# Kernel tuning notes

Measured on AMD Instinct MI355X. Metric: run time of the kernel, lower is better.

The kernel has to match this reference:

```python
import jax, jax.numpy as jnp
import numpy as np

B, S, H = 4, 2048, 1024

def setup_inputs() -> dict:
    key = jax.random.key(0)
    ks = jax.random.split(key, 7)
    scale = 1.0 / np.sqrt(H)
    x  = jax.random.normal(ks[0], (B, S, H), dtype=jnp.float32)
    Wq = jax.random.normal(ks[1], (H, H), dtype=jnp.float32) * scale
    bq = jax.random.normal(ks[2], (H,), dtype=jnp.float32) * 0.01
    Wk = jax.random.normal(ks[3], (H, H), dtype=jnp.float32) * scale
    bk = jax.random.normal(ks[4], (H,), dtype=jnp.float32) * 0.01
    Wv = jax.random.normal(ks[5], (H, H), dtype=jnp.float32) * scale
    bv = jax.random.normal(ks[6], (H,), dtype=jnp.float32) * 0.01
    return {"x": x, "Wq": Wq, "bq": bq, "Wk": Wk, "bk": bk, "Wv": Wv, "bv": bv}

def reference(x, Wq, bq, Wk, bk, Wv, bv):
    # q/k/v: [B, S, H]
    q = jnp.einsum('bsh,hd->bsd', x, Wq.T) + bq
    k = jnp.einsum('bsh,hd->bsd', x, Wk.T) + bk
    v = jnp.einsum('bsh,hd->bsd', x, Wv.T) + bv
    # NOTE: original module applies NO 1/sqrt(H) scaling.
    scores = jnp.einsum('bqd,bkd->bqk', q, k)  # [B, S, S]
    attn = jax.nn.softmax(scores, axis=-1)
    return jnp.einsum('bqk,bkd->bqd', attn, v)  # [B, S, H]
```

## Files before the change

kernel.cpp:

```cpp
#include <hip/hip_runtime.h>
#include <hip/hip_bf16.h>


typedef __attribute__((ext_vector_type(4))) float f32x4;
typedef __attribute__((ext_vector_type(16))) float f32x16;
typedef __attribute__((ext_vector_type(8))) _Float16 f16x8;
typedef __attribute__((ext_vector_type(4))) unsigned short us4;
typedef __attribute__((ext_vector_type(8))) unsigned short us8;

#define MFMA16F(a, b, c) __builtin_amdgcn_mfma_f32_16x16x32_f16((a), (b), (c), 0, 0, 0)
#define MFMA32F(a, b, c) __builtin_amdgcn_mfma_f32_32x32x16_f16((a), (b), (c), 0, 0, 0)

static __device__ __forceinline__ unsigned short f2h_u(float x) {
  _Float16 h = (_Float16)x;
  return *reinterpret_cast<unsigned short*>(&h);
}
static __device__ __forceinline__ float hu2f(unsigned short u) {
  _Float16 h;
  *reinterpret_cast<unsigned short*>(&h) = u;
  return (float)h;
}

__global__ __launch_bounds__(256) void split_x_kernel(
    const float* __restrict__ in, unsigned short* __restrict__ outp, int ntiles) {
  const int t = blockIdx.x * 256 + threadIdx.x;
  if (t >= ntiles * 64) return;
  const int tile = t >> 6;
  const int l = t & 63;
  const int m = (tile >> 5) * 16 + (l & 15);
  const int kb = (tile & 31) * 32 + (l >> 4) * 8;
  const float* src = in + (size_t)m * 1024 + kb;
  f32x4 v0 = *(const f32x4*)src;
  f32x4 v1 = *(const f32x4*)(src + 4);
  us8 h;
#pragma unroll
  for (int j = 0; j < 4; j++) {
    h[j] = f2h_u(v0[j]);
    h[j + 4] = f2h_u(v1[j]);
  }
  *(us8*)(outp + (size_t)tile * 512 + l * 8) = h;
}

__global__ __launch_bounds__(256) void split3_kernel(
    const float* __restrict__ w0, const float* __restrict__ w1,
    const float* __restrict__ w2,
    unsigned short* __restrict__ h0, unsigned short* __restrict__ l0,
    unsigned short* __restrict__ h1, unsigned short* __restrict__ l1,
    unsigned short* __restrict__ h2, unsigned short* __restrict__ l2) {
  const int which = blockIdx.y;
  const float* in = which == 0 ? w0 : (which == 1 ? w1 : w2);
  unsigned short* hi = which == 0 ? h0 : (which == 1 ? h1 : h2);
  unsigned short* lo = which == 0 ? l0 : (which == 1 ? l1 : l2);
  const int t = blockIdx.x * 256 + threadIdx.x;
  const int tile = t >> 6;
  const int l = t & 63;
  const int m = (tile >> 5) * 16 + (l & 15);
  const int kb = (tile & 31) * 32 + (l >> 4) * 8;
  const float* src = in + (size_t)m * 1024 + kb;
  f32x4 v0 = *(const f32x4*)src;
  f32x4 v1 = *(const f32x4*)(src + 4);
  us8 h, lv;
#pragma unroll
  for (int j = 0; j < 4; j++) {
    unsigned short hu = f2h_u(v0[j]);
    h[j] = hu;
    lv[j] = f2h_u(v0[j] - hu2f(hu));
    hu = f2h_u(v1[j]);
    h[j + 4] = hu;
    lv[j + 4] = f2h_u(v1[j] - hu2f(hu));
  }
  *(us8*)(hi + (size_t)tile * 512 + l * 8) = h;
  if (which != 2) *(us8*)(lo + (size_t)tile * 512 + l * 8) = lv;
}

__global__ __launch_bounds__(256, 2) void proj_fused_kernel(
    const unsigned short* __restrict__ Xf,
    const unsigned short* __restrict__ Wqh, const unsigned short* __restrict__ Wql,
    const unsigned short* __restrict__ Wkh, const unsigned short* __restrict__ Wkl,
    const unsigned short* __restrict__ Wvh,
    const float* __restrict__ bq, const float* __restrict__ bk,
    const float* __restrict__ bv,
    unsigned short* __restrict__ Qf, unsigned short* __restrict__ Kf,
    unsigned short* __restrict__ Vt) {
  const int tid = threadIdx.x;
  const int lane = tid & 63;
  const int wid = tid >> 6;
  const int lrow = lane & 15;
  const int kg = lane >> 4;
  const int bx = blockIdx.x;
  const int ntb = blockIdx.y * 16 + wid * 4;
  const int z = blockIdx.z;

  const unsigned short* Wh = z == 0 ? Wqh : (z == 1 ? Wkh : Wvh);
  const unsigned short* Wl = z == 0 ? Wql : Wkl;
  const float* bias = z == 0 ? bq : (z == 1 ? bk : bv);

  const unsigned short* xf = Xf + (size_t)(bx * 8) * 32 * 512 + lane * 8;

  f32x4 acc[8][4];
#pragma unroll
  for (int mf = 0; mf < 8; mf++)
#pragma unroll
    for (int cf = 0; cf < 4; cf++) acc[mf][cf] = f32x4{0.f, 0.f, 0.f, 0.f};

  if (z < 2) {
    for (int kt = 0; kt < 32; kt++) {
      const size_t o = (size_t)kt * 512;
      f16x8 ah[8];
#pragma unroll
      for (int mf = 0; mf < 8; mf++)
        ah[mf] = *(const f16x8*)(xf + (size_t)mf * 32 * 512 + o);
#pragma unroll
      for (int cf = 0; cf < 4; cf++) {
        const size_t wo = ((size_t)(ntb + cf) * 32 + kt) * 512 + lane * 8;
        f16x8 bh = *(const f16x8*)(Wh + wo);
        f16x8 bl = *(const f16x8*)(Wl + wo);
#pragma unroll
        for (int mf = 0; mf < 8; mf++) {
          acc[mf][cf] = MFMA16F(ah[mf], bh, acc[mf][cf]);
          acc[mf][cf] = MFMA16F(ah[mf], bl, acc[mf][cf]);
        }
      }
    }
    unsigned short* O = z == 0 ? Qf : Kf;
    const int b = bx >> 4;
#pragma unroll
    for (int mf = 0; mf < 8; mf++) {
      const int s0 = (bx & 15) * 128 + mf * 16 + kg * 4;
#pragma unroll
      for (int cf = 0; cf < 4; cf++) {
        const int nt = ntb + cf;
        const float bv_ = bias[nt * 16 + lrow];
#pragma unroll
        for (int i = 0; i < 4; i++) {
          const int s = s0 + i;
          const size_t a = ((size_t)((b * 64 + (s >> 5)) * 64 + nt)) * 512 +
                           (s & 31) * 16 + lrow;
          O[a] = f2h_u(acc[mf][cf][i] + bv_);
        }
      }
    }
  } else {
    for (int kt = 0; kt < 32; kt++) {
      const size_t o = (size_t)kt * 512;
      f16x8 ah[8];
#pragma unroll
      for (int mf = 0; mf < 8; mf++)
        ah[mf] = *(const f16x8*)(xf + (size_t)mf * 32 * 512 + o);
#pragma unroll
      for (int cf = 0; cf < 4; cf++) {
        const size_t wo = ((size_t)(ntb + cf) * 32 + kt) * 512 + lane * 8;
        f16x8 bh = *(const f16x8*)(Wh + wo);
#pragma unroll
        for (int mf = 0; mf < 8; mf++) acc[mf][cf] = MFMA16F(ah[mf], bh, acc[mf][cf]);
      }
    }
    const int b = bx >> 4;
#pragma unroll
    for (int mf = 0; mf < 8; mf++) {
      const int kl_hi = (bx & 15) * 8 + mf;
#pragma unroll
      for (int cf = 0; cf < 4; cf++) {
        const int d = (ntb + cf) * 16 + lrow;
        const float bv_ = bias[d];
        us4 pk;
#pragma unroll
        for (int i = 0; i < 4; i++) pk[i] = f2h_u(acc[mf][cf][i] + bv_);
        const size_t a = ((size_t)(b * 32 + (d >> 5)) * 128 + kl_hi) * 512 +
                         (size_t)(d & 31) * 16 + kg * 4;
        *reinterpret_cast<us4*>(&Vt[a]) = pk;
      }
    }
  }
}

__global__ __launch_bounds__(1024, 4) void attn_kernel(
    const unsigned short* __restrict__ Qf, const unsigned short* __restrict__ Kf,
    const unsigned short* __restrict__ Vt, float* __restrict__ out) {
  __shared__ unsigned short LDSB[65536];
  __shared__ float redM[16][32];
  __shared__ float redS[16][32];
  __shared__ float rowinv[32];

  const int tid = threadIdx.x;
  const int lane = tid & 63;
  const int wid = tid >> 6;
  const int lq = lane & 31;
  const int hi = lane >> 5;
  const int lo16 = lq * 16 + hi * 8;

  const int id = blockIdx.x;
  const int xcd = id & 7;
  const int b = xcd >> 1;
  const int qt = (xcd & 1) + ((id >> 3) << 1);
  const int q0 = qt * 32;

  {
    const unsigned short* qsrc = Qf + ((size_t)(b * 64 + qt) * 64) * 512;
#pragma unroll
    for (int i = 0; i < 4; i++) {
      const int idx = (i * 1024 + tid) * 8;
      *(us8*)&LDSB[idx] = *(const us8*)&qsrc[idx];
    }
  }
  __syncthreads();

  f32x16 acc0, acc1, acc2, acc3;
#pragma unroll
  for (int r = 0; r < 16; r++) { acc0[r] = 0.f; acc1[r] = 0.f; acc2[r] = 0.f; acc3[r] = 0.f; }

  const unsigned short* kb = Kf + ((size_t)(b * 64 + wid * 4) * 64) * 512 + lo16;
#define KLD(G, KKK) (*(const f16x8*)(kb + (size_t)(G)*64 * 512 + (size_t)(KKK)*512))
  f16x8 kc0 = KLD(0, 0), kc1 = KLD(1, 0), kc2 = KLD(2, 0), kc3 = KLD(3, 0);
  for (int kk = 0; kk < 63; kk++) {
    f16x8 q = *(const f16x8*)&LDSB[kk * 512 + lo16];
    f16x8 kn0 = KLD(0, kk + 1), kn1 = KLD(1, kk + 1),
          kn2 = KLD(2, kk + 1), kn3 = KLD(3, kk + 1);
    __builtin_amdgcn_s_setprio(1);
    acc0 = MFMA32F(kc0, q, acc0);
    acc1 = MFMA32F(kc1, q, acc1);
    acc2 = MFMA32F(kc2, q, acc2);
    acc3 = MFMA32F(kc3, q, acc3);
    __builtin_amdgcn_s_setprio(0);
    kc0 = kn0; kc1 = kn1; kc2 = kn2; kc3 = kn3;
  }
  {
    f16x8 q = *(const f16x8*)&LDSB[63 * 512 + lo16];
    acc0 = MFMA32F(kc0, q, acc0);
    acc1 = MFMA32F(kc1, q, acc1);
    acc2 = MFMA32F(kc2, q, acc2);
    acc3 = MFMA32F(kc3, q, acc3);
  }
#undef KLD

  float m = -3.0e38f;
#pragma unroll
  for (int r = 0; r < 16; r++) {
    m = fmaxf(m, fmaxf(fmaxf(acc0[r], acc1[r]), fmaxf(acc2[r], acc3[r])));
  }
  m = fmaxf(m, __shfl_xor(m, 32));
  if (hi == 0) redM[wid][lq] = m;
  __syncthreads();
  float M = redM[0][lq];
#pragma unroll
  for (int w = 1; w < 16; w++) M = fmaxf(M, redM[w][lq]);

  float s = 0.f;
#pragma unroll
  for (int r = 0; r < 16; r++) {
    acc0[r] = __expf(acc0[r] - M); s += acc0[r];
    acc1[r] = __expf(acc1[r] - M); s += acc1[r];
    acc2[r] = __expf(acc2[r] - M); s += acc2[r];
    acc3[r] = __expf(acc3[r] - M); s += acc3[r];
  }
  s += __shfl_xor(s, 32);
  if (hi == 0) redS[wid][lq] = s;
  __syncthreads();
  if (tid < 32) {
    float ss = 0.f;
#pragma unroll
    for (int w = 0; w < 16; w++) ss += redS[w][tid];
    rowinv[tid] = 1.0f / ss;
  }

  const int swz = (lq & 7) << 3;
  const int pb = lq * 2048 + wid * 128 + 4 * hi;
#define PWRITE(GG, ACC)                                                     \
  {                                                                         \
    _Pragma("unroll")                                                       \
    for (int qd = 0; qd < 4; qd++) {                                        \
      us4 pk;                                                               \
      _Pragma("unroll")                                                     \
      for (int i = 0; i < 4; i++) pk[i] = f2h_u(ACC[qd * 4 + i]);           \
      *(us4*)&LDSB[(pb + (GG)*32 + qd * 8) ^ swz] = pk;                     \
    }                                                                       \
  }
  PWRITE(0, acc0)
  PWRITE(1, acc1)
  PWRITE(2, acc2)
  PWRITE(3, acc3)
#undef PWRITE
  __syncthreads();

  f32x16 o0, o1;
#pragma unroll
  for (int r = 0; r < 16; r++) { o0[r] = 0.f; o1[r] = 0.f; }

  const unsigned short* vt0 = Vt + ((size_t)(b * 32 + wid * 2) * 128) * 512 + lo16;
  const unsigned short* vt1 = vt0 + (size_t)128 * 512;
  const int prow = lq * 2048 + hi * 8;
#define VLD(P, KKK) (*(const f16x8*)((P) + (size_t)(KKK)*512))
  f16x8 vc0 = VLD(vt0, 0), vc1 = VLD(vt1, 0);
  for (int kk = 0; kk < 127; kk++) {
    f16x8 pa = *(const f16x8*)&LDSB[(prow + kk * 16) ^ swz];
    f16x8 vn0 = VLD(vt0, kk + 1), vn1 = VLD(vt1, kk + 1);
    __builtin_amdgcn_s_setprio(1);
    o0 = MFMA32F(pa, vc0, o0);
    o1 = MFMA32F(pa, vc1, o1);
    __builtin_amdgcn_s_setprio(0);
    vc0 = vn0; vc1 = vn1;
  }
  {
    f16x8 pa = *(const f16x8*)&LDSB[(prow + 127 * 16) ^ swz];
    o0 = MFMA32F(pa, vc0, o0);
    o1 = MFMA32F(pa, vc1, o1);
  }
#undef VLD

  float rv[16];
#pragma unroll
  for (int r = 0; r < 16; r++) rv[r] = rowinv[(r & 3) + 8 * (r >> 2) + 4 * hi];
  const int d0 = wid * 64 + lq;
#pragma unroll
  for (int r = 0; r < 16; r++) {
    const int q = (r & 3) + 8 * (r >> 2) + 4 * hi;
    const size_t ob = ((size_t)b * 2048 + q0 + q) * 1024;
    out[ob + d0] = o0[r] * rv[r];
    out[ob + d0 + 32] = o1[r] * rv[r];
  }
}

extern "C" void kernel_launch(void* const* d_in, const int* in_sizes, int n_in,
                              void* d_out, int out_size, void* d_ws, size_t ws_size,
                              hipStream_t stream) {
  const float* x  = (const float*)d_in[0];
  const float* Wq = (const float*)d_in[1];
  const float* bq = (const float*)d_in[2];
  const float* Wk = (const float*)d_in[3];
  const float* bk = (const float*)d_in[4];
  const float* Wv = (const float*)d_in[5];
  const float* bv = (const float*)d_in[6];
  float* o = (float*)d_out;

  const size_t NX = (size_t)8192 * 1024;
  const size_t NW = (size_t)1024 * 1024;
  unsigned short* p = (unsigned short*)d_ws;
  unsigned short* Xf = p; p += NX;
  unsigned short* Qf = p; p += NX;
  unsigned short* Kf = p; p += NX;
  unsigned short* Vt = p; p += NX;
  unsigned short* Wqh = p; p += NW;
  unsigned short* Wql = p; p += NW;
  unsigned short* Wkh = p; p += NW;
  unsigned short* Wkl = p; p += NW;
  unsigned short* Wvh = p; p += NW;
  unsigned short* Wvl = p; p += NW;

  split_x_kernel<<<4096, 256, 0, stream>>>(x, Xf, 16384);
  dim3 gs(512, 3);
  split3_kernel<<<gs, 256, 0, stream>>>(Wq, Wk, Wv, Wqh, Wql, Wkh, Wkl, Wvh, Wvl);

  dim3 gp(64, 4, 3), bp(256);
  proj_fused_kernel<<<gp, bp, 0, stream>>>(Xf, Wqh, Wql, Wkh, Wkl, Wvh,
                                           bq, bk, bv, Qf, Kf, Vt);

  attn_kernel<<<256, 1024, 0, stream>>>(Qf, Kf, Vt, o);
}
```

Before: 187.4 us.

## Split attention over key halves with 64-query tiles and a combine kernel

Each attention block now handles 64 queries against half of the keys, so every K and V fragment it loads feeds two MFMAs. Partial outputs are written as fp16 along with per-row max and sum, and a new combine kernel merges the two halves with softmax rescaling. This is meant to halve the global K/V traffic per query. In exchange it adds an fp16 partial-output round trip through memory, an extra kernel launch, and more accumulator registers per thread.

```diff
diff --git a/kernel.cpp b/kernel.cpp
--- a/kernel.cpp
+++ b/kernel.cpp
@@ -174,13 +174,13 @@
   }
 }
 
-__global__ __launch_bounds__(1024, 4) void attn_kernel(
+__global__ __launch_bounds__(1024, 1) void attn_part_kernel(
     const unsigned short* __restrict__ Qf, const unsigned short* __restrict__ Kf,
-    const unsigned short* __restrict__ Vt, float* __restrict__ out) {
+    const unsigned short* __restrict__ Vt, unsigned short* __restrict__ Opart,
+    float* __restrict__ Mpart, float* __restrict__ Lpart) {
   __shared__ unsigned short LDSB[65536];
-  __shared__ float redM[16][32];
-  __shared__ float redS[16][32];
-  __shared__ float rowinv[32];
+  __shared__ float redM[16][64];
+  __shared__ float redS[16][64];
 
   const int tid = threadIdx.x;
   const int lane = tid & 63;
@@ -192,132 +192,177 @@
   const int id = blockIdx.x;
   const int xcd = id & 7;
   const int b = xcd >> 1;
-  const int qt = (xcd & 1) + ((id >> 3) << 1);
-  const int q0 = qt * 32;
+  const int kh = xcd & 1;
+  const int qt = id >> 3;
 
   {
-    const unsigned short* qsrc = Qf + ((size_t)(b * 64 + qt) * 64) * 512;
-#pragma unroll
-    for (int i = 0; i < 4; i++) {
-      const int idx = (i * 1024 + tid) * 8;
-      *(us8*)&LDSB[idx] = *(const us8*)&qsrc[idx];
+    const us8* qsrc = (const us8*)(Qf + ((size_t)(b * 64 + qt * 2) * 64) * 512);
+    us8* qdst = (us8*)LDSB;
+#pragma unroll
+    for (int i = 0; i < 8; i++) {
+      const int u = i * 1024 + tid;
+      const int kk = u >> 7, rem = u & 127;
+      qdst[u] = qsrc[(rem >> 6) * 4096 + kk * 64 + (rem & 63)];
     }
   }
   __syncthreads();
 
-  f32x16 acc0, acc1, acc2, acc3;
-#pragma unroll
-  for (int r = 0; r < 16; r++) { acc0[r] = 0.f; acc1[r] = 0.f; acc2[r] = 0.f; acc3[r] = 0.f; }
-
-  const unsigned short* kb = Kf + ((size_t)(b * 64 + wid * 4) * 64) * 512 + lo16;
+  f32x16 s00, s01, s10, s11;
+#pragma unroll
+  for (int r = 0; r < 16; r++) { s00[r] = 0.f; s01[r] = 0.f; s10[r] = 0.f; s11[r] = 0.f; }
+
+  const unsigned short* kb =
+      Kf + ((size_t)(b * 64 + kh * 32 + wid * 2) * 64) * 512 + lo16;
 #define KLD(G, KKK) (*(const f16x8*)(kb + (size_t)(G)*64 * 512 + (size_t)(KKK)*512))
-  f16x8 kc0 = KLD(0, 0), kc1 = KLD(1, 0), kc2 = KLD(2, 0), kc3 = KLD(3, 0);
+  f16x8 kc0 = KLD(0, 0), kc1 = KLD(1, 0);
   for (int kk = 0; kk < 63; kk++) {
-    f16x8 q = *(const f16x8*)&LDSB[kk * 512 + lo16];
-    f16x8 kn0 = KLD(0, kk + 1), kn1 = KLD(1, kk + 1),
-          kn2 = KLD(2, kk + 1), kn3 = KLD(3, kk + 1);
+    f16x8 qA = *(const f16x8*)&LDSB[kk * 1024 + lo16];
+    f16x8 qB = *(const f16x8*)&LDSB[kk * 1024 + 512 + lo16];
+    f16x8 kn0 = KLD(0, kk + 1), kn1 = KLD(1, kk + 1);
     __builtin_amdgcn_s_setprio(1);
-    acc0 = MFMA32F(kc0, q, acc0);
-    acc1 = MFMA32F(kc1, q, acc1);
-    acc2 = MFMA32F(kc2, q, acc2);
-    acc3 = MFMA32F(kc3, q, acc3);
+    s00 = MFMA32F(kc0, qA, s00);
+    s01 = MFMA32F(kc0, qB, s01);
+    s10 = MFMA32F(kc1, qA, s10);
+    s11 = MFMA32F(kc1, qB, s11);
     __builtin_amdgcn_s_setprio(0);
-    kc0 = kn0; kc1 = kn1; kc2 = kn2; kc3 = kn3;
+    kc0 = kn0; kc1 = kn1;
   }
   {
-    f16x8 q = *(const f16x8*)&LDSB[63 * 512 + lo16];
-    acc0 = MFMA32F(kc0, q, acc0);
-    acc1 = MFMA32F(kc1, q, acc1);
-    acc2 = MFMA32F(kc2, q, acc2);
-    acc3 = MFMA32F(kc3, q, acc3);
+    f16x8 qA = *(const f16x8*)&LDSB[63 * 1024 + lo16];
+    f16x8 qB = *(const f16x8*)&LDSB[63 * 1024 + 512 + lo16];
+    s00 = MFMA32F(kc0, qA, s00);
+    s01 = MFMA32F(kc0, qB, s01);
+    s10 = MFMA32F(kc1, qA, s10);
+    s11 = MFMA32F(kc1, qB, s11);
   }
 #undef KLD
 
-  float m = -3.0e38f;
+  float mA = -3.0e38f, mB = -3.0e38f;
 #pragma unroll
   for (int r = 0; r < 16; r++) {
-    m = fmaxf(m, fmaxf(fmaxf(acc0[r], acc1[r]), fmaxf(acc2[r], acc3[r])));
-  }
-  m = fmaxf(m, __shfl_xor(m, 32));
-  if (hi == 0) redM[wid][lq] = m;
+    mA = fmaxf(mA, fmaxf(s00[r], s10[r]));
+    mB = fmaxf(mB, fmaxf(s01[r], s11[r]));
+  }
+  mA = fmaxf(mA, __shfl_xor(mA, 32));
+  mB = fmaxf(mB, __shfl_xor(mB, 32));
+  if (hi == 0) { redM[wid][lq] = mA; redM[wid][32 + lq] = mB; }
   __syncthreads();
-  float M = redM[0][lq];
-#pragma unroll
-  for (int w = 1; w < 16; w++) M = fmaxf(M, redM[w][lq]);
-
-  float s = 0.f;
+  float MA = redM[0][lq], MB = redM[0][32 + lq];
+#pragma unroll
+  for (int w = 1; w < 16; w++) {
+    MA = fmaxf(MA, redM[w][lq]);
+    MB = fmaxf(MB, redM[w][32 + lq]);
+  }
+  float sA = 0.f, sB = 0.f;
 #pragma unroll
   for (int r = 0; r < 16; r++) {
-    acc0[r] = __expf(acc0[r] - M); s += acc0[r];
-    acc1[r] = __expf(acc1[r] - M); s += acc1[r];
-    acc2[r] = __expf(acc2[r] - M); s += acc2[r];
-    acc3[r] = __expf(acc3[r] - M); s += acc3[r];
-  }
-  s += __shfl_xor(s, 32);
-  if (hi == 0) redS[wid][lq] = s;
+    s00[r] = __expf(s00[r] - MA); sA += s00[r];
+    s10[r] = __expf(s10[r] - MA); sA += s10[r];
+    s01[r] = __expf(s01[r] - MB); sB += s01[r];
+    s11[r] = __expf(s11[r] - MB); sB += s11[r];
+  }
+  sA += __shfl_xor(sA, 32);
+  sB += __shfl_xor(sB, 32);
+  if (hi == 0) { redS[wid][lq] = sA; redS[wid][32 + lq] = sB; }
+
+  const int swz = (lq & 7) << 3;
+#define PW(ACC, QQ, KB)                                                       \
+  {                                                                           \
+    _Pragma("unroll")                                                         \
+    for (int qd = 0; qd < 4; qd++) {                                          \
+      us4 pk;                                                                 \
+      _Pragma("unroll")                                                       \
+      for (int i = 0; i < 4; i++) pk[i] = f2h_u(ACC[qd * 4 + i]);             \
+      *(us4*)&LDSB[(((QQ)*1024) + (KB) + qd * 8 + 4 * hi) ^ swz] = pk;        \
+    }                                                                         \
+  }
+  PW(s00, lq, wid * 64)
+  PW(s01, 32 + lq, wid * 64)
+  PW(s10, lq, wid * 64 + 32)
+  PW(s11, 32 + lq, wid * 64 + 32)
+#undef PW
   __syncthreads();
-  if (tid < 32) {
-    float ss = 0.f;
-#pragma unroll
-    for (int w = 0; w < 16; w++) ss += redS[w][tid];
-    rowinv[tid] = 1.0f / ss;
-  }
-
-  const int swz = (lq & 7) << 3;
-  const int pb = lq * 2048 + wid * 128 + 4 * hi;
-#define PWRITE(GG, ACC)                                                     \
-  {                                                                         \
-    _Pragma("unroll")                                                       \
-    for (int qd = 0; qd < 4; qd++) {                                        \
-      us4 pk;                                                               \
-      _Pragma("unroll")                                                     \
-      for (int i = 0; i < 4; i++) pk[i] = f2h_u(ACC[qd * 4 + i]);           \
-      *(us4*)&LDSB[(pb + (GG)*32 + qd * 8) ^ swz] = pk;                     \
-    }                                                                       \
-  }
-  PWRITE(0, acc0)
-  PWRITE(1, acc1)
-  PWRITE(2, acc2)
-  PWRITE(3, acc3)
-#undef PWRITE
-  __syncthreads();
-
-  f32x16 o0, o1;
-#pragma unroll
-  for (int r = 0; r < 16; r++) { o0[r] = 0.f; o1[r] = 0.f; }
-
-  const unsigned short* vt0 = Vt + ((size_t)(b * 32 + wid * 2) * 128) * 512 + lo16;
-  const unsigned short* vt1 = vt0 + (size_t)128 * 512;
-  const int prow = lq * 2048 + hi * 8;
-#define VLD(P, KKK) (*(const f16x8*)((P) + (size_t)(KKK)*512))
-  f16x8 vc0 = VLD(vt0, 0), vc1 = VLD(vt1, 0);
-  for (int kk = 0; kk < 127; kk++) {
-    f16x8 pa = *(const f16x8*)&LDSB[(prow + kk * 16) ^ swz];
-    f16x8 vn0 = VLD(vt0, kk + 1), vn1 = VLD(vt1, kk + 1);
+
+  if (tid < 64) {
+    float M = redM[0][tid], L = redS[0][tid];
+#pragma unroll
+    for (int w = 1; w < 16; w++) {
+      M = fmaxf(M, redM[w][tid]);
+      L += redS[w][tid];
+    }
+    const size_t gi = (size_t)(b * 2 + kh) * 2048 + qt * 64 + tid;
+    Mpart[gi] = M;
+    Lpart[gi] = L;
+  }
+
+  f32x16 o00, o01, o10, o11;
+#pragma unroll
+  for (int r = 0; r < 16; r++) { o00[r] = 0.f; o01[r] = 0.f; o10[r] = 0.f; o11[r] = 0.f; }
+
+  const unsigned short* vb =
+      Vt + ((size_t)((b * 32 + wid * 2) * 128) + kh * 64) * 512 + lo16;
+#define VLD(G, KKK) (*(const f16x8*)(vb + (size_t)(G)*128 * 512 + (size_t)(KKK)*512))
+  f16x8 vc0 = VLD(0, 0), vc1 = VLD(1, 0);
+  const int prA = lq * 1024 + hi * 8;
+  const int prB = (32 + lq) * 1024 + hi * 8;
+  for (int kk = 0; kk < 63; kk++) {
+    f16x8 paA = *(const f16x8*)&LDSB[(prA + kk * 16) ^ swz];
+    f16x8 paB = *(const f16x8*)&LDSB[(prB + kk * 16) ^ swz];
+    f16x8 vn0 = VLD(0, kk + 1), vn1 = VLD(1, kk + 1);
     __builtin_amdgcn_s_setprio(1);
-    o0 = MFMA32F(pa, vc0, o0);
-    o1 = MFMA32F(pa, vc1, o1);
+    o00 = MFMA32F(paA, vc0, o00);
+    o01 = MFMA32F(paA, vc1, o01);
+    o10 = MFMA32F(paB, vc0, o10);
+    o11 = MFMA32F(paB, vc1, o11);
     __builtin_amdgcn_s_setprio(0);
     vc0 = vn0; vc1 = vn1;
   }
   {
-    f16x8 pa = *(const f16x8*)&LDSB[(prow + 127 * 16) ^ swz];
-    o0 = MFMA32F(pa, vc0, o0);
-    o1 = MFMA32F(pa, vc1, o1);
+    f16x8 paA = *(const f16x8*)&LDSB[(prA + 63 * 16) ^ swz];
+    f16x8 paB = *(const f16x8*)&LDSB[(prB + 63 * 16) ^ swz];
+    o00 = MFMA32F(paA, vc0, o00);
+    o01 = MFMA32F(paA, vc1, o01);
+    o10 = MFMA32F(paB, vc0, o10);
+    o11 = MFMA32F(paB, vc1, o11);
   }
 #undef VLD
 
-  float rv[16];
-#pragma unroll
-  for (int r = 0; r < 16; r++) rv[r] = rowinv[(r & 3) + 8 * (r >> 2) + 4 * hi];
+  unsigned short* ob = Opart + ((size_t)(b * 2 + kh) * 2048 + qt * 64) * 1024;
   const int d0 = wid * 64 + lq;
 #pragma unroll
   for (int r = 0; r < 16; r++) {
-    const int q = (r & 3) + 8 * (r >> 2) + 4 * hi;
-    const size_t ob = ((size_t)b * 2048 + q0 + q) * 1024;
-    out[ob + d0] = o0[r] * rv[r];
-    out[ob + d0 + 32] = o1[r] * rv[r];
-  }
+    const int crow = (r & 3) + 8 * (r >> 2) + 4 * hi;
+    ob[(size_t)crow * 1024 + d0] = f2h_u(o00[r]);
+    ob[(size_t)crow * 1024 + d0 + 32] = f2h_u(o01[r]);
+    ob[(size_t)(crow + 32) * 1024 + d0] = f2h_u(o10[r]);
+    ob[(size_t)(crow + 32) * 1024 + d0 + 32] = f2h_u(o11[r]);
+  }
+}
+
+__global__ __launch_bounds__(256) void attn_combine_kernel(
+    const unsigned short* __restrict__ Opart, const float* __restrict__ Mpart,
+    const float* __restrict__ Lpart, float* __restrict__ out) {
+  const int t = blockIdx.x * 256 + threadIdx.x;
+  const int row = t >> 7;
+  const int dd = (t & 127) * 8;
+  const int b = row >> 11, sl = row & 2047;
+  const int i0 = (b * 2) * 2048 + sl, i1 = i0 + 2048;
+  const float m0 = Mpart[i0], m1 = Mpart[i1];
+  const float M = fmaxf(m0, m1);
+  float w0 = __expf(m0 - M), w1 = __expf(m1 - M);
+  const float inv = 1.0f / (w0 * Lpart[i0] + w1 * Lpart[i1]);
+  w0 *= inv; w1 *= inv;
+  const us8 o0 = *(const us8*)&Opart[(size_t)i0 * 1024 + dd];
+  const us8 o1 = *(const us8*)&Opart[(size_t)i1 * 1024 + dd];
+  float* op = out + (size_t)row * 1024 + dd;
+  f32x4 r0, r1;
+#pragma unroll
+  for (int j = 0; j < 4; j++) {
+    r0[j] = w0 * hu2f(o0[j]) + w1 * hu2f(o1[j]);
+    r1[j] = w0 * hu2f(o0[j + 4]) + w1 * hu2f(o1[j + 4]);
+  }
+  *(f32x4*)op = r0;
+  *(f32x4*)(op + 4) = r1;
 }
 
 extern "C" void kernel_launch(void* const* d_in, const int* in_sizes, int n_in,
@@ -345,6 +390,9 @@
   unsigned short* Wkl = p; p += NW;
   unsigned short* Wvh = p; p += NW;
   unsigned short* Wvl = p; p += NW;
+  unsigned short* Opart = p; p += 2 * NX;
+  float* Mpart = (float*)p; p += 32768;
+  float* Lpart = (float*)p; p += 32768;
 
   split_x_kernel<<<4096, 256, 0, stream>>>(x, Xf, 16384);
   dim3 gs(512, 3);
@@ -354,5 +402,6 @@
   proj_fused_kernel<<<gp, bp, 0, stream>>>(Xf, Wqh, Wql, Wkh, Wkl, Wvh,
                                            bq, bk, bv, Qf, Kf, Vt);
 
-  attn_kernel<<<256, 1024, 0, stream>>>(Qf, Kf, Vt, o);
-}
+  attn_part_kernel<<<256, 1024, 0, stream>>>(Qf, Kf, Vt, Opart, Mpart, Lpart);
+  attn_combine_kernel<<<4096, 256, 0, stream>>>(Opart, Mpart, Lpart, o);
+}
```

Result: no change. 183.9 us (-1.9%).
